# Optimization experiments

Hardware: AMD Instinct MI355X
Metric: run time of the kernel (lower is better)

Reference implementation:

```python
import jax, jax.numpy as jnp
import numpy as np
from jax import lax

EPS = 1e-5
K = 16

def bn(x, g, b):
    # BatchNorm2d in training mode: biased batch stats over (B,H,W)
    m = x.mean(axis=(0, 2, 3), keepdims=True)
    v = x.var(axis=(0, 2, 3), keepdims=True)
    return (x - m) * lax.rsqrt(v + EPS) * g.reshape(1, -1, 1, 1) + b.reshape(1, -1, 1, 1)

def lrelu(x):
    return jnp.where(x >= 0, x, 0.01 * x)

def conv1x1(x, w, b):  # x:[B,C,N,K], w:[O,C]
    return jnp.einsum('bcnk,oc->bonk', x, w) + b.reshape(1, -1, 1, 1)

def edge_features_xyz(x, pc, k):
    B, C, N = x.shape
    xt = jnp.swapaxes(x, 1, 2)                      # [B,N,C]
    xs = jnp.sum(xt * xt, axis=2, keepdims=True)    # [B,N,1]
    dist = -2.0 * jnp.einsum('bnc,bcm->bnm', xt, x) + xs + jnp.swapaxes(xs, 1, 2)
    idx = jnp.argsort(dist, axis=2)[:, :, 1:k + 1]  # [B,N,k] skip self
    gather = jax.vmap(lambda fb, ib: fb[:, ib])     # [C,N],[N,k]->[C,N,k]
    nb = gather(x, idx)                             # [B,C,N,k]
    nb_xyz = gather(pc, idx)                        # [B,3,N,k]
    central = jnp.broadcast_to(x[..., None], (B, C, N, k))
    central_xyz = jnp.broadcast_to(pc[..., None], (B, 3, N, k))
    e_fea = jnp.concatenate([central, nb - central], axis=1)          # [B,2C,N,k]
    e_xyz = jnp.concatenate([central_xyz, nb_xyz - central_xyz], axis=1)  # [B,6,N,k]
    return e_fea, e_xyz

def forward(x, pc, fea_w, fea_b, fea_g, fea_be, xyz_w, xyz_b, xyz_g, xyz_be,
            all1_w, all1_b, all1_g, all1_be, all2_w, all2_b, all2_g, all2_be,
            inte_w, inte_b, inte_g, inte_be, c2_w, c2_b, c2_g, c2_be):
    B, Fin, N = x.shape
    k = K
    e_fea, e_xyz = edge_features_xyz(x, pc, k)      # [B,2Fin,N,k],[B,6,N,k]
    w_fea = lrelu(bn(conv1x1(e_fea, fea_w, fea_b), fea_g, fea_be))   # [B,16,N,k]
    w_xyz = lrelu(bn(conv1x1(e_xyz, xyz_w, xyz_b), xyz_g, xyz_be))   # [B,16,N,k]
    w = w_fea * w_xyz
    w = lrelu(bn(conv1x1(w, all1_w, all1_b), all1_g, all1_be))       # [B,64,N,k]
    w = lrelu(bn(conv1x1(w, all2_w, all2_b), all2_g, all2_be))       # [B,2Fin,N,k]
    w = jax.nn.softmax(w, axis=-1)
    CC = 2 * Fin
    # inte_conv_hk: Conv2d(2Fin->4Fin, kernel [1, k//2+1]) -> [B,4Fin,N,k//2]
    inte = lax.conv_general_dilated(e_fea, inte_w, (1, 1), 'VALID',
                                    dimension_numbers=('NCHW', 'OIHW', 'NCHW'))
    inte = inte + inte_b.reshape(1, -1, 1, 1)
    inte = lrelu(bn(inte, inte_g, inte_be))
    # torch reshape dance: [B,4Fin,N,k/2] -> [B,N,4Fin,k/2] -> [B,N,2Fin,2,k/2] -> [B,N,2Fin,k] -> [B,2Fin,N,k]
    inte = jnp.transpose(inte, (0, 2, 1, 3)).reshape(B, N, CC, 2, k // 2)
    inte = inte.reshape(B, N, CC, k).transpose(0, 2, 1, 3)
    inte_x = inte * w
    merge = jnp.concatenate([e_fea, inte_x], axis=3)                 # [B,2Fin,N,2k]
    # conv2: kernel [1,2k] spans full width -> contraction
    out = jnp.einsum('bcnw,ocw->bon', merge, c2_w[:, :, 0, :]) + c2_b.reshape(1, -1, 1)
    out = out[..., None]                                             # [B,2Fout,N,1]
    out = jnp.maximum(bn(out, c2_g, c2_be), 0.0)                     # ReLU
    Fout = out.shape[1] // 2
    return out.reshape(B, Fout, 2 * N)

def setup_inputs():
    B, Fin, Fout, N, k = 8, 64, 64, 2048, 16
    ks = jax.random.split(jax.random.key(0), 10)
    p = lambda i, s, sc=0.05: jax.random.normal(ks[i], s, jnp.float32) * sc
    return {
        'x': p(0, (B, Fin, N), 1.0),
        'pc': p(1, (B, 3, N), 1.0),
        'fea_w': p(2, (16, 2 * Fin)), 'fea_b': jnp.zeros(16), 'fea_g': jnp.ones(16), 'fea_be': jnp.zeros(16),
        'xyz_w': p(3, (16, 6)), 'xyz_b': jnp.zeros(16), 'xyz_g': jnp.ones(16), 'xyz_be': jnp.zeros(16),
        'all1_w': p(4, (64, 16)), 'all1_b': jnp.zeros(64), 'all1_g': jnp.ones(64), 'all1_be': jnp.zeros(64),
        'all2_w': p(5, (2 * Fin, 64)), 'all2_b': jnp.zeros(2 * Fin), 'all2_g': jnp.ones(2 * Fin), 'all2_be': jnp.zeros(2 * Fin),
        'inte_w': p(6, (4 * Fin, 2 * Fin, 1, k // 2 + 1)), 'inte_b': jnp.zeros(4 * Fin), 'inte_g': jnp.ones(4 * Fin), 'inte_be': jnp.zeros(4 * Fin),
        'c2_w': p(7, (2 * Fout, 2 * Fin, 1, 2 * k)), 'c2_b': jnp.zeros(2 * Fout), 'c2_g': jnp.ones(2 * Fout), 'c2_be': jnp.zeros(2 * Fout),
    }

def reference(x, pc, fea_w, fea_b, fea_g, fea_be, xyz_w, xyz_b, xyz_g, xyz_be,
              all1_w, all1_b, all1_g, all1_be, all2_w, all2_b, all2_g, all2_be,
              inte_w, inte_b, inte_g, inte_be, c2_w, c2_b, c2_g, c2_be):
    return forward(x, pc, fea_w, fea_b, fea_g, fea_be, xyz_w, xyz_b, xyz_g, xyz_be,
                   all1_w, all1_b, all1_g, all1_be, all2_w, all2_b, all2_g, all2_be,
                   inte_w, inte_b, inte_g, inte_be, c2_w, c2_b, c2_g, c2_be)
```

## Files before the change

kernel.cpp:

```cpp
#include <hip/hip_runtime.h>
#include <math.h>

typedef unsigned short ushort_t;

#define B_   8
#define N_   2048
#define K_   16
#define C2_  128
#define C4_  256
#define KH_  8
#define TAP_ 9
#define NK_  32768
#define EPSv 1e-5f
#define BIGF 3.0e38f
#define NMASK 2047

constexpr size_t AL(size_t x) { return (x + 255) & ~(size_t)255; }
constexpr size_t OFF_XT   = 0;
constexpr size_t OFF_IDX  = OFF_XT  + AL(4ull * B_ * N_ * 64);
constexpr size_t OFF_U1   = OFF_IDX + AL(4ull * B_ * N_ * K_);
constexpr size_t OFF_V1   = OFF_U1  + AL(4ull * B_ * 16 * N_);
constexpr size_t OFF_U2   = OFF_V1  + AL(4ull * B_ * N_ * 16);
constexpr size_t OFF_V2   = OFF_U2  + AL(4ull * B_ * 16 * N_);
constexpr size_t OFF_S    = OFF_V2  + AL(4ull * B_ * N_ * 16);
constexpr size_t OFF_P    = OFF_S   + AL(4ull * B_ * N_ * C2_);
constexpr size_t OFF_W1   = OFF_P   + AL(4ull * B_ * N_ * C4_);
constexpr size_t OFF_QB   = OFF_W1  + AL(4ull * B_ * 16 * NK_);
constexpr size_t OFF_ITB  = OFF_QB  + AL(2ull * (size_t)B_ * N_ * TAP_ * C4_);
constexpr size_t OFF_A4B  = OFF_ITB + AL(2ull * (size_t)B_ * N_ * 2048);
constexpr size_t OFF_M    = OFF_A4B + AL(2ull * (size_t)B_ * N_ * 2048);
constexpr size_t OFF_PART = OFF_M   + AL(2ull * (size_t)B_ * N_ * 2048);
constexpr size_t OFF_OUT2 = OFF_PART+ AL(4ull * 2 * (size_t)B_ * N_ * C2_);
constexpr size_t OFF_WQ2  = OFF_OUT2+ AL(4ull * B_ * N_ * C2_);
constexpr size_t OFF_WC2  = OFF_WQ2 + AL(4ull * TAP_ * C4_ * 64);
constexpr size_t OFF_WP2  = OFF_WC2 + AL(4ull * 3072 * C2_);
constexpr size_t OFF_WS2  = OFF_WP2 + AL(4ull * C4_ * 64);
constexpr size_t OFF_WU12 = OFF_WS2 + AL(4ull * C2_ * 64);
constexpr size_t OFF_WV12 = OFF_WU12+ AL(4ull * 16 * 64);
constexpr size_t OFF_WU22 = OFF_WV12+ AL(4ull * 16 * 64);
constexpr size_t OFF_WV22 = OFF_WU22+ AL(4ull * 64);
constexpr size_t OFF_A12  = OFF_WV22+ AL(4ull * 64);
constexpr size_t OFF_A22  = OFF_A12 + AL(4ull * 64 * 16);
constexpr size_t OFF_ST   = OFF_A22 + AL(4ull * C2_ * 64);
constexpr size_t OFF_PROG = OFF_ST  + AL(4ull * 4096);
constexpr size_t POOL_SZ  = OFF_PROG + AL(4ull * 64);

static char* g_pool_mem = nullptr;
struct PoolInit {
  PoolInit() { if (hipMalloc((void**)&g_pool_mem, POOL_SZ) != hipSuccess) g_pool_mem = nullptr; }
};
static PoolInit g_pool_init;

#define ST_S1S 0
#define ST_S1Q 16
#define ST_S2S 32
#define ST_S2Q 48
#define ST_S5S 64
#define ST_S5Q 320
#define ST_S4S 576
#define ST_S4Q 704
#define ST_S6S 832
#define ST_S6Q 960
#define ST_B1SC 1088
#define ST_B1SH 1104
#define ST_B2SC 1120
#define ST_B2SH 1136
#define ST_B3SC 1152
#define ST_B3SH 1216
#define ST_B4SC 1280
#define ST_B4SH 1408
#define ST_B5SC 1536
#define ST_B5SH 1792
#define ST_B6SC 2048
#define ST_B6SH 2176
#define ST_S3M  2304
#define ST_S3V  2440

#define BASE(b)  char* bb = (b)
#define P_XT   ((float*)(bb + OFF_XT))
#define P_IDX  ((int*)(bb + OFF_IDX))
#define P_U1   ((float*)(bb + OFF_U1))
#define P_V1   ((float*)(bb + OFF_V1))
#define P_U2   ((float*)(bb + OFF_U2))
#define P_V2   ((float*)(bb + OFF_V2))
#define P_Sb   ((float*)(bb + OFF_S))
#define P_P    ((float*)(bb + OFF_P))
#define P_W1   ((float*)(bb + OFF_W1))
#define P_QB   ((ushort_t*)(bb + OFF_QB))
#define P_IT   ((ushort_t*)(bb + OFF_ITB))
#define P_A4   ((ushort_t*)(bb + OFF_A4B))
#define P_M    ((ushort_t*)(bb + OFF_M))
#define P_PART ((float*)(bb + OFF_PART))
#define P_OUT2 ((float*)(bb + OFF_OUT2))
#define P_WQ2  ((float*)(bb + OFF_WQ2))
#define P_WC2  ((float*)(bb + OFF_WC2))
#define P_WP2  ((float*)(bb + OFF_WP2))
#define P_WS2  ((float*)(bb + OFF_WS2))
#define P_WU12 ((float*)(bb + OFF_WU12))
#define P_WV12 ((float*)(bb + OFF_WV12))
#define P_WU22 ((float*)(bb + OFF_WU22))
#define P_WV22 ((float*)(bb + OFF_WV22))
#define P_A12  ((float*)(bb + OFF_A12))
#define P_A22  ((float*)(bb + OFF_A22))
#define P_ST   ((float*)(bb + OFF_ST))
#define P_PROG ((int*)(bb + OFF_PROG))

#define PROG(id) do { if (threadIdx.x == 0) atomicAdd(&P_PROG[(id)], 1); } while (0)

static __device__ __forceinline__ float lrelu(float x) { return x >= 0.0f ? x : 0.01f * x; }
static __device__ __forceinline__ float bf2f(unsigned h) {
  union { float f; unsigned u; } v; v.u = h << 16; return v.f;
}
static __device__ __forceinline__ ushort_t f2bf(float f) {
  union { float f; unsigned u; } v; v.f = f;
  unsigned r = v.u + 0x7fffu + ((v.u >> 16) & 1u);
  return (ushort_t)(r >> 16);
}

__global__ __launch_bounds__(256) void zero_kernel(char* base)
{
  BASE(base);
  for (int i = threadIdx.x; i < 4096; i += 256) P_ST[i] = 0.0f;
  for (int i = threadIdx.x; i < 64; i += 256) P_PROG[i] = 0;
  __syncthreads();
  if (threadIdx.x == 0) P_PROG[0] = 1;
}

__global__ __launch_bounds__(256) void xt_kernel(char* base, const float* __restrict__ x)
{
  BASE(base);
  PROG(8);
  int b = blockIdx.x >> 5; int m0 = (blockIdx.x & 31) * 64;
  int t = threadIdx.x;
  __shared__ float tile[64 * 65];
  for (int i = t; i < 4096; i += 256) {
    int ml = i & 63, c = i >> 6;
    tile[c * 65 + ml] = x[((size_t)(b * 64 + c)) * N_ + m0 + ml];
  }
  __syncthreads();
  for (int i = t; i < 4096; i += 256) {
    int c = i & 63, ml = i >> 6;
    P_XT[((size_t)(b * N_) + m0 + ml) * 64 + c] = tile[c * 65 + ml];
  }
}

__global__ __launch_bounds__(256) void prep_kernel(char* base,
    const float* __restrict__ fea_w,
    const float* __restrict__ xyz_w, const float* __restrict__ inte_w,
    const float* __restrict__ c2_w, const float* __restrict__ all1_w,
    const float* __restrict__ all2_w)
{
  BASE(base);
  PROG(1);
  int i = blockIdx.x * 256 + threadIdx.x;
  if (i < 1024) { int o = i & 15, c = i >> 4;
    P_WU12[i] = fea_w[o * 128 + c] - fea_w[o * 128 + 64 + c]; return; }
  i -= 1024;
  if (i < 1024) { int o = i & 15, c = i >> 4;
    P_WV12[i] = fea_w[o * 128 + 64 + c]; return; }
  i -= 1024;
  if (i < 64) { int c = i & 3, o = i >> 2;
    P_WU22[i] = (c < 3) ? (xyz_w[o * 6 + c] - xyz_w[o * 6 + 3 + c]) : 0.0f; return; }
  i -= 64;
  if (i < 64) { int c = i & 3, o = i >> 2;
    P_WV22[i] = (c < 3) ? xyz_w[o * 6 + 3 + c] : 0.0f; return; }
  i -= 64;
  if (i < 16384) { int o = i & 255, c = i >> 8;
    float s = 0.0f;
    for (int t = 0; t < TAP_; t++)
      s += inte_w[(o * 128 + c) * TAP_ + t] - inte_w[(o * 128 + 64 + c) * TAP_ + t];
    P_WP2[i] = s; return; }
  i -= 16384;
  if (i < 147456) {
    int o = i & 255; int tc = i >> 8; int c = tc & 63; int tt = tc >> 6;
    P_WQ2[i] = inte_w[(o * 128 + 64 + c) * TAP_ + tt]; return; }
  i -= 147456;
  if (i < 8192) { int o = i & 127, c = i >> 7;
    float s = 0.0f;
    for (int p = 0; p < 16; p++)
      s += c2_w[(o * 128 + c) * 32 + p] - c2_w[(o * 128 + 64 + c) * 32 + p];
    P_WS2[i] = s; return; }
  i -= 8192;
  if (i < 393216) { int o = i & 127; int k = i >> 7; float v;
    if (k < 1024) { int c = k >> 4, p = k & 15; v = c2_w[(o * 128 + 64 + c) * 32 + p]; }
    else { int kr = k - 1024; int cc = kr >> 4, kk = kr & 15; v = c2_w[(o * 128 + cc) * 32 + 16 + kk]; }
    P_WC2[i] = v; return; }
  i -= 393216;
  if (i < 1024) { int c = i & 15, o = i >> 4; P_A12[i] = all1_w[o * 16 + c]; return; }
  i -= 1024;
  if (i < 8192) {
    int o = i & 127, c = i >> 7; P_A22[i] = all2_w[o * 64 + c]; return; }
}

__global__ __launch_bounds__(256) void phaseA_kernel(char* base,
                                                     const float* __restrict__ x,
                                                     const float* __restrict__ pc)
{
  BASE(base);
  PROG(2);
  __shared__ __align__(16) char smem[33824];
  int bid = blockIdx.x;
  int t = threadIdx.x;
  if (bid % 5 != 0) {
    int kb = bid - bid / 5 - 1;
    int b = kb >> 9; int n0 = (kb & 511) * 4;
    float (*sdist)[N_] = (float(*)[N_])smem;
    float (*xn)[64]    = (float(*)[64])(smem + 32768);
    float* sxn         = (float*)(smem + 32768 + 1024);
    {
      int nn = t >> 6, c = t & 63;
      xn[nn][c] = P_XT[((size_t)(b * N_) + n0 + nn) * 64 + c];
    }
    __syncthreads();
    if (t < 4) {
      float s = 0.0f;
      for (int c = 0; c < 64; c++) { float v = xn[t][c]; s += v * v; }
      sxn[t] = s;
    }
    __syncthreads();
    float dd[32]; float xs[8];
#pragma unroll
    for (int i = 0; i < 32; i++) dd[i] = 0.0f;
#pragma unroll
    for (int i = 0; i < 8; i++) xs[i] = 0.0f;
    const float* xbase = x + (size_t)b * 64 * N_ + (t << 3);
    for (int cq = 0; cq < 16; cq++) {
      float4 a0 = *(const float4*)&xn[0][cq * 4];
      float4 a1 = *(const float4*)&xn[1][cq * 4];
      float4 a2 = *(const float4*)&xn[2][cq * 4];
      float4 a3 = *(const float4*)&xn[3][cq * 4];
      float p[4][8];
#pragma unroll
      for (int cc = 0; cc < 4; cc++) {
        const float* xr = xbase + (size_t)(cq * 4 + cc) * N_;
        float4 u = *(const float4*)xr;
        float4 v = *(const float4*)(xr + 4);
        p[cc][0] = u.x; p[cc][1] = u.y; p[cc][2] = u.z; p[cc][3] = u.w;
        p[cc][4] = v.x; p[cc][5] = v.y; p[cc][6] = v.z; p[cc][7] = v.w;
      }
#pragma unroll
      for (int j = 0; j < 8; j++) {
        float x0 = p[0][j], x1 = p[1][j], x2 = p[2][j], x3 = p[3][j];
        xs[j] += x0 * x0 + x1 * x1 + x2 * x2 + x3 * x3;
        dd[0 * 8 + j] += a0.x * x0 + a0.y * x1 + a0.z * x2 + a0.w * x3;
        dd[1 * 8 + j] += a1.x * x0 + a1.y * x1 + a1.z * x2 + a1.w * x3;
        dd[2 * 8 + j] += a2.x * x0 + a2.y * x1 + a2.z * x2 + a2.w * x3;
        dd[3 * 8 + j] += a3.x * x0 + a3.y * x1 + a3.z * x2 + a3.w * x3;
      }
    }
    float sx0 = sxn[0], sx1 = sxn[1], sx2 = sxn[2], sx3 = sxn[3];
    int mb = t << 3;
#pragma unroll
    for (int j = 0; j < 8; j++) {
      int m = mb + j;
      float d0 = -2.0f * dd[0 * 8 + j] + sx0 + xs[j];
      float d1 = -2.0f * dd[1 * 8 + j] + sx1 + xs[j];
      float d2 = -2.0f * dd[2 * 8 + j] + sx2 + xs[j];
      float d3 = -2.0f * dd[3 * 8 + j] + sx3 + xs[j];
      sdist[0][m] = (m == n0 + 0) ? BIGF : d0;
      sdist[1][m] = (m == n0 + 1) ? BIGF : d1;
      sdist[2][m] = (m == n0 + 2) ? BIGF : d2;
      sdist[3][m] = (m == n0 + 3) ? BIGF : d3;
    }
    __syncthreads();
    int ln = t & 63; int wv = t >> 6;
    float v[32];
#pragma unroll
    for (int j = 0; j < 32; j++) v[j] = sdist[wv][ln + j * 64];
    float bv = v[0]; int bj = 0;
#pragma unroll
    for (int j = 1; j < 32; j++) { if (v[j] < bv) { bv = v[j]; bj = j; } }
    int* op = P_IDX + ((size_t)(b * N_) + n0 + wv) * K_;
    for (int it = 0; it < K_; it++) {
      float rv = bv; int ri = ln + (bj << 6);
#pragma unroll
      for (int off = 32; off > 0; off >>= 1) {
        float ov = __shfl_xor(rv, off);
        int oi = __shfl_xor(ri, off);
        if (ov < rv || (ov == rv && oi < ri)) { rv = ov; ri = oi; }
      }
      if (ln == 0) op[it] = ri;
      if ((ri & 63) == ln) {
        int slot = ri >> 6;
#pragma unroll
        for (int j = 0; j < 32; j++) v[j] = (j == slot) ? BIGF : v[j];
        bv = v[0]; bj = 0;
#pragma unroll
        for (int j = 1; j < 32; j++) { if (v[j] < bv) { bv = v[j]; bj = j; } }
      }
    }
    return;
  }
  int s = bid / 5;
  if (s < 512) {
    int b = s >> 6; int m0 = (s & 63) * 32;
    float (*actS)[40] = (float(*)[40])smem;
    float (*pcs)[32]  = (float(*)[32])(smem + 10240);
    for (int i = t; i < 2048; i += 256) {
      int c = i & 63, mm = i >> 6;
      actS[c][mm] = P_XT[((size_t)(b * N_) + m0 + mm) * 64 + c];
    }
    if (t < 96) {
      int c = t >> 5, mm = t & 31;
      pcs[c][mm] = pc[(b * 3 + c) * N_ + m0 + mm];
    }
    __syncthreads();
    size_t bN = (size_t)(b * N_);
    {
      int og = t & 31, pg = t >> 5;
      float acc[8][4];
#pragma unroll
      for (int oi = 0; oi < 8; oi++)
#pragma unroll
        for (int pj = 0; pj < 4; pj++) acc[oi][pj] = 0.0f;
      for (int c = 0; c < 64; c++) {
        float4 a = *(const float4*)&actS[c][pg * 4];
        const float* wr = P_WP2 + c * 256 + og * 8;
        float4 w0 = *(const float4*)wr;
        float4 w1 = *(const float4*)(wr + 4);
        float av[4] = {a.x, a.y, a.z, a.w};
        float wv[8] = {w0.x, w0.y, w0.z, w0.w, w1.x, w1.y, w1.z, w1.w};
#pragma unroll
        for (int oi = 0; oi < 8; oi++)
#pragma unroll
          for (int pj = 0; pj < 4; pj++) acc[oi][pj] += wv[oi] * av[pj];
      }
#pragma unroll
      for (int pj = 0; pj < 4; pj++) {
        float* pp = P_P + (bN + m0 + pg * 4 + pj) * C4_ + og * 8;
        *(float4*)pp = make_float4(acc[0][pj], acc[1][pj], acc[2][pj], acc[3][pj]);
        *(float4*)(pp + 4) = make_float4(acc[4][pj], acc[5][pj], acc[6][pj], acc[7][pj]);
      }
    }
    {
      int og = t & 15, pg = t >> 4;
      float acc[8][2];
#pragma unroll
      for (int oi = 0; oi < 8; oi++) { acc[oi][0] = 0.0f; acc[oi][1] = 0.0f; }
      for (int c = 0; c < 64; c++) {
        float a0 = actS[c][pg * 2], a1 = actS[c][pg * 2 + 1];
        const float* wr = P_WS2 + c * 128 + og * 8;
        float4 w0 = *(const float4*)wr;
        float4 w1 = *(const float4*)(wr + 4);
        float wv[8] = {w0.x, w0.y, w0.z, w0.w, w1.x, w1.y, w1.z, w1.w};
#pragma unroll
        for (int oi = 0; oi < 8; oi++) { acc[oi][0] += wv[oi] * a0; acc[oi][1] += wv[oi] * a1; }
      }
#pragma unroll
      for (int pj = 0; pj < 2; pj++) {
        float* sp = P_Sb + (bN + m0 + pg * 2 + pj) * C2_ + og * 8;
        *(float4*)sp = make_float4(acc[0][pj], acc[1][pj], acc[2][pj], acc[3][pj]);
        *(float4*)(sp + 4) = make_float4(acc[4][pj], acc[5][pj], acc[6][pj], acc[7][pj]);
      }
    }
    {
      int o = t & 15, pg = t >> 4;
      float aU[2] = {0.0f, 0.0f}, aV[2] = {0.0f, 0.0f};
      for (int c = 0; c < 64; c++) {
        float wu = P_WU12[c * 16 + o];
        float wv = P_WV12[c * 16 + o];
        float a0 = actS[c][pg * 2], a1 = actS[c][pg * 2 + 1];
        aU[0] += wu * a0; aU[1] += wu * a1;
        aV[0] += wv * a0; aV[1] += wv * a1;
      }
      float u0 = P_WU22[o * 4], u1 = P_WU22[o * 4 + 1], u2w = P_WU22[o * 4 + 2];
      float v0 = P_WV22[o * 4], v1 = P_WV22[o * 4 + 1], v2w = P_WV22[o * 4 + 2];
#pragma unroll
      for (int pj = 0; pj < 2; pj++) {
        int m = m0 + pg * 2 + pj;
        P_U1[((b * 16 + o) << 11) + m] = aU[pj];
        P_V1[(bN + m) * 16 + o] = aV[pj];
        float p0 = pcs[0][pg * 2 + pj], p1 = pcs[1][pg * 2 + pj], p2 = pcs[2][pg * 2 + pj];
        P_U2[((b * 16 + o) << 11) + m] = u0 * p0 + u1 * p1 + u2w * p2;
        P_V2[(bN + m) * 16 + o] = v0 * p0 + v1 * p1 + v2w * p2;
      }
    }
    return;
  }
  {
    int q = s - 512;
    int b = q >> 6; int m0 = (q & 63) * 32;
    float (*actS)[40] = (float(*)[40])smem;
    for (int i = t; i < 2048; i += 256) {
      int c = i & 63, mm = i >> 6;
      actS[c][mm] = P_XT[((size_t)(b * N_) + m0 + mm) * 64 + c];
    }
    __syncthreads();
    int og = t & 31;
    int pg = t >> 5;
    int m = m0 + pg * 4;
    for (int t9 = 0; t9 < TAP_; t9++) {
      const float* wbase = P_WQ2 + ((size_t)t9 * 64) * 256 + og * 8;
      float acc[8][4];
#pragma unroll
      for (int oi = 0; oi < 8; oi++)
#pragma unroll
        for (int pj = 0; pj < 4; pj++) acc[oi][pj] = 0.0f;
      for (int kc = 0; kc < 64; kc++) {
        float4 a = *(const float4*)&actS[kc][pg * 4];
        const float* wr = wbase + (size_t)kc * 256;
        float4 w0 = *(const float4*)wr;
        float4 w1 = *(const float4*)(wr + 4);
        float av[4] = {a.x, a.y, a.z, a.w};
        float wv[8] = {w0.x, w0.y, w0.z, w0.w, w1.x, w1.y, w1.z, w1.w};
#pragma unroll
        for (int oi = 0; oi < 8; oi++)
#pragma unroll
          for (int pj = 0; pj < 4; pj++)
            acc[oi][pj] += wv[oi] * av[pj];
      }
#pragma unroll
      for (int pj = 0; pj < 4; pj++) {
        ushort_t* qp = P_QB + ((size_t)(b * N_ + m + pj) * TAP_ + t9) * C4_ + og * 8;
        unsigned u0 = (unsigned)f2bf(acc[0][pj]) | ((unsigned)f2bf(acc[1][pj]) << 16);
        unsigned u1 = (unsigned)f2bf(acc[2][pj]) | ((unsigned)f2bf(acc[3][pj]) << 16);
        unsigned u2 = (unsigned)f2bf(acc[4][pj]) | ((unsigned)f2bf(acc[5][pj]) << 16);
        unsigned u3 = (unsigned)f2bf(acc[6][pj]) | ((unsigned)f2bf(acc[7][pj]) << 16);
        *(uint4*)qp = make_uint4(u0, u1, u2, u3);
      }
    }
    return;
  }
}

__global__ __launch_bounds__(256) void phaseB_kernel(char* base,
                                                     const float* __restrict__ inte_b,
                                                     const float* __restrict__ fea_b,
                                                     const float* __restrict__ xyz_b)
{
  BASE(base);
  PROG(15);
  __shared__ __align__(16) char smem[1024];
  int bid = blockIdx.x;
  int t = threadIdx.x;
  if (bid % 5 != 0) {
    int kb = bid - bid / 5 - 1;
    int b = kb >> 9; int n0 = (kb & 511) * 4;
    int o = t;
    int (*sidx)[16] = (int(*)[16])smem;
    if (t < 64) sidx[t >> 4][t & 15] = P_IDX[((size_t)(b * N_) + n0 + (t >> 4)) * K_ + (t & 15)] & NMASK;
    __syncthreads();
    float bias = inte_b[o];
    float ssum = 0.0f, ssq = 0.0f;
    for (int nn = 0; nn < 4; nn++) {
      int n = n0 + nn;
      float bse = bias + P_P[((size_t)(b * N_) + n) * C4_ + o];
      float acc[8];
#pragma unroll
      for (int j = 0; j < 8; j++) acc[j] = bse;
      for (int p = 0; p < 16; p++) {
        const ushort_t* qr = P_QB + (size_t)(b * N_ + sidx[nn][p]) * TAP_ * C4_ + o;
#pragma unroll
        for (int tt = 0; tt < TAP_; tt++) {
          int j = p - tt;
          if (j >= 0 && j < 8) acc[j] += bf2f(((unsigned)qr[tt * C4_]) << 16 >> 16 << 16 >> 16);
        }
      }
      ushort_t* ip = P_IT + ((size_t)(b * N_) + n) * 2048 + o * 8;
#pragma unroll
      for (int j = 0; j < 8; j++) { float v = acc[j]; ip[j] = f2bf(v); ssum += v; ssq += v * v; }
    }
    atomicAdd(&P_ST[ST_S5S + o], ssum);
    atomicAdd(&P_ST[ST_S5Q + o], ssq);
    return;
  }
  {
    int s = bid / 5;
    int b = s >> 7; int n0 = (s & 127) * 16;
    int o = t & 15; int kk = t >> 4;
    float* red = (float*)smem;
    float fb = fea_b[o], xb = xyz_b[o];
    float s1 = 0, q1 = 0, s2 = 0, q2 = 0;
    for (int nn = 0; nn < 16; nn++) {
      int n = n0 + nn;
      int m = P_IDX[((b << 11) + n) * K_ + kk] & NMASK;
      float a1 = fb + P_U1[((b * 16 + o) << 11) + n] + P_V1[(((size_t)(b << 11) + m) << 4) + o];
      s1 += a1; q1 += a1 * a1;
      float a2 = xb + P_U2[((b * 16 + o) << 11) + n] + P_V2[(((size_t)(b << 11) + m) << 4) + o];
      s2 += a2; q2 += a2 * a2;
    }
    red[t] = s1; __syncthreads();
    if (t < 16) { float s = 0; for (int k2 = 0; k2 < 16; k2++) s += red[k2 * 16 + t]; atomicAdd(&P_ST[ST_S1S + t], s); }
    __syncthreads();
    red[t] = q1; __syncthreads();
    if (t < 16) { float s = 0; for (int k2 = 0; k2 < 16; k2++) s += red[k2 * 16 + t]; atomicAdd(&P_ST[ST_S1Q + t], s); }
    __syncthreads();
    red[t] = s2; __syncthreads();
    if (t < 16) { float s = 0; for (int k2 = 0; k2 < 16; k2++) s += red[k2 * 16 + t]; atomicAdd(&P_ST[ST_S2S + t], s); }
    __syncthreads();
    red[t] = q2; __syncthreads();
    if (t < 16) { float s = 0; for (int k2 = 0; k2 < 16; k2++) s += red[k2 * 16 + t]; atomicAdd(&P_ST[ST_S2Q + t], s); }
    return;
  }
}

__global__ __launch_bounds__(256) void finalize_bn_kernel(char* base,
                                   const float* __restrict__ g,
                                   const float* __restrict__ be,
                                   int sum_off, int sq_off, int sc_off, int sh_off,
                                   int nch, float inv_cnt, int kid)
{
  BASE(base);
  PROG(kid);
  int i = threadIdx.x;
  if (i < nch) {
    float mu = P_ST[sum_off + i] * inv_cnt;
    float var = fmaxf(P_ST[sq_off + i] * inv_cnt - mu * mu, 0.0f);
    float s = g[i] * rsqrtf(var + EPSv);
    P_ST[sc_off + i] = s; P_ST[sh_off + i] = be[i] - mu * s;
  }
}

__global__ __launch_bounds__(256) void w1_kernel(char* base,
    const float* __restrict__ fea_b, const float* __restrict__ xyz_b)
{
  BASE(base);
  PROG(7);
  int b = blockIdx.x >> 7; int n0 = (blockIdx.x & 127) * 16;
  int t = threadIdx.x;
  __shared__ int sidx[16 * 16];
  __shared__ __align__(16) float ol[16 * 260];
  {
    int nl = t >> 4, k = t & 15;
    sidx[nl * 16 + k] = P_IDX[((size_t)((b << 11) + n0 + nl)) * 16 + k] & NMASK;
  }
  __syncthreads();
  int c = t >> 4; int nl = t & 15; int n = n0 + nl;
  float u1 = P_U1[((b * 16 + c) << 11) + n];
  float u2 = P_U2[((b * 16 + c) << 11) + n];
  float c1 = fea_b[c] + u1, c2v = xyz_b[c] + u2;
  float s1 = P_ST[ST_B1SC + c], h1 = P_ST[ST_B1SH + c];
  float s2 = P_ST[ST_B2SC + c], h2 = P_ST[ST_B2SH + c];
  float o16[16];
#pragma unroll
  for (int kk = 0; kk < 16; kk++) {
    int m = sidx[nl * 16 + kk];
    float a1 = c1 + P_V1[(((size_t)(b << 11) + m) << 4) + c];
    a1 = lrelu(a1 * s1 + h1);
    float a2 = c2v + P_V2[(((size_t)(b << 11) + m) << 4) + c];
    a2 = lrelu(a2 * s2 + h2);
    o16[kk] = a1 * a2;
  }
  float* wp = P_W1 + ((size_t)(b * 16 + c)) * NK_ + ((size_t)n << 4);
#pragma unroll
  for (int j = 0; j < 4; j++)
    *(float4*)(wp + j * 4) = make_float4(o16[4 * j], o16[4 * j + 1], o16[4 * j + 2], o16[4 * j + 3]);
  float* orow = ol + c * 260 + nl * 16;
#pragma unroll
  for (int j = 0; j < 4; j++)
    *(float4*)(orow + j * 4) = make_float4(o16[4 * j], o16[4 * j + 1], o16[4 * j + 2], o16[4 * j + 3]);
  __syncthreads();
  if (t < 136) {
    int cc1 = 0, rem = t;
    while (rem >= 16 - cc1) { rem -= 16 - cc1; cc1++; }
    int cc2 = cc1 + rem;
    const float* r1 = ol + cc1 * 260;
    const float* r2 = ol + cc2 * 260;
    float acc = 0.0f;
    for (int e = 0; e < 256; e += 4) {
      float4 xv = *(const float4*)(r1 + e);
      float4 yv = *(const float4*)(r2 + e);
      acc += xv.x * yv.x + xv.y * yv.y + xv.z * yv.z + xv.w * yv.w;
    }
    atomicAdd(&P_ST[ST_S3M + t], acc);
  } else if (t < 152) {
    const float* r = ol + (t - 136) * 260;
    float acc = 0.0f;
    for (int e = 0; e < 256; e += 4) {
      float4 xv = *(const float4*)(r + e);
      acc += xv.x + xv.y + xv.z + xv.w;
    }
    atomicAdd(&P_ST[ST_S3V + t - 136], acc);
  }
}

__global__ __launch_bounds__(256) void finalize_bn3_kernel(char* base,
                                    const float* __restrict__ b1,
                                    const float* __restrict__ g,
                                    const float* __restrict__ be)
{
  BASE(base);
  PROG(9);
  int o = threadIdx.x;
  if (o >= 64) return;
  float A[16];
  for (int c = 0; c < 16; c++) A[c] = P_A12[o * 16 + c];
  float dv = 0.0f;
  for (int c = 0; c < 16; c++) dv += A[c] * P_ST[ST_S3V + c];
  float quad = 0.0f; int p = 0;
  for (int c1 = 0; c1 < 16; c1++)
    for (int c2 = c1; c2 < 16; c2++) {
      float m = P_ST[ST_S3M + p]; p++;
      quad += (c1 == c2 ? 1.0f : 2.0f) * A[c1] * A[c2] * m;
    }
  float bo = b1[o];
  const float inv = 1.0f / 262144.0f;
  float mean = dv * inv + bo;
  float e2 = quad * inv + 2.0f * bo * dv * inv + bo * bo;
  float var = fmaxf(e2 - mean * mean, 0.0f);
  float s = g[o] * rsqrtf(var + EPSv);
  P_ST[ST_B3SC + o] = s; P_ST[ST_B3SH + o] = be[o] - mean * s;
}

__global__ __launch_bounds__(256) void a4_kernel(char* base,
                                                 const float* __restrict__ all1_b,
                                                 const float* __restrict__ all2_b)
{
  BASE(base);
  PROG(10);
  int b = blockIdx.x >> 9; int col0 = (blockIdx.x & 511) * 64;
  int t = threadIdx.x;
  __shared__ float sw[16 * 68];
  __shared__ __align__(16) float hS[64 * 68];
  for (int i = t; i < 1024; i += 256) {
    int c = i >> 6, l = i & 63;
    sw[c * 68 + l] = P_W1[((size_t)(b * 16 + c)) * NK_ + col0 + l];
  }
  __syncthreads();
  {
    int col = t & 63; int q = t >> 6;
    float in16[16];
#pragma unroll
    for (int c = 0; c < 16; c++) in16[c] = sw[c * 68 + col];
    for (int oo = 0; oo < 16; oo++) {
      int o = q * 16 + oo;
      const float* wr = P_A12 + o * 16;
      float a = all1_b[o];
#pragma unroll
      for (int c = 0; c < 16; c++) a += wr[c] * in16[c];
      hS[o * 68 + col] = lrelu(a * P_ST[ST_B3SC + o] + P_ST[ST_B3SH + o]);
    }
  }
  __syncthreads();
  int cg = t & 15;
  int og = t >> 4;
  float acc[8][4];
#pragma unroll
  for (int oi = 0; oi < 8; oi++) {
    float bo = all2_b[og * 8 + oi];
#pragma unroll
    for (int cj = 0; cj < 4; cj++) acc[oi][cj] = bo;
  }
  for (int hk = 0; hk < 64; hk++) {
    float4 hv = *(const float4*)&hS[hk * 68 + cg * 4];
    const float* wr = P_A22 + hk * 128 + og * 8;
    float4 w0 = *(const float4*)wr;
    float4 w1 = *(const float4*)(wr + 4);
    float av[4] = {hv.x, hv.y, hv.z, hv.w};
    float wv[8] = {w0.x, w0.y, w0.z, w0.w, w1.x, w1.y, w1.z, w1.w};
#pragma unroll
    for (int oi = 0; oi < 8; oi++)
#pragma unroll
      for (int cj = 0; cj < 4; cj++)
        acc[oi][cj] += wv[oi] * av[cj];
  }
  int colb = col0 + cg * 4;
  int n = colb >> 4; int kk0 = colb & 15;
  ushort_t* dst = P_A4 + ((size_t)(b * N_) + n) * 2048 + kk0;
  float psum[8], qsum[8];
#pragma unroll
  for (int oi = 0; oi < 8; oi++) {
    int o = og * 8 + oi;
    unsigned lo = (unsigned)f2bf(acc[oi][0]) | ((unsigned)f2bf(acc[oi][1]) << 16);
    unsigned hi = (unsigned)f2bf(acc[oi][2]) | ((unsigned)f2bf(acc[oi][3]) << 16);
    *(uint2*)(dst + o * 16) = make_uint2(lo, hi);
    float r0 = bf2f(lo & 0xffffu), r1 = bf2f(lo >> 16);
    float r2 = bf2f(hi & 0xffffu), r3 = bf2f(hi >> 16);
    psum[oi] = r0 + r1 + r2 + r3;
    qsum[oi] = r0 * r0 + r1 * r1 + r2 * r2 + r3 * r3;
  }
  __syncthreads();
  float* redS = hS;
#pragma unroll
  for (int oi = 0; oi < 8; oi++) redS[(og * 8 + oi) * 16 + cg] = psum[oi];
  __syncthreads();
  if (t < 128) {
    float s = 0.0f;
    for (int j = 0; j < 16; j++) s += redS[t * 16 + j];
    atomicAdd(&P_ST[ST_S4S + t], s);
  }
  __syncthreads();
#pragma unroll
  for (int oi = 0; oi < 8; oi++) redS[(og * 8 + oi) * 16 + cg] = qsum[oi];
  __syncthreads();
  if (t < 128) {
    float s = 0.0f;
    for (int j = 0; j < 16; j++) s += redS[t * 16 + j];
    atomicAdd(&P_ST[ST_S4Q + t], s);
  }
}

__global__ __launch_bounds__(256) void softfuse_kernel(char* base)
{
  BASE(base);
  PROG(13);
  int rid = blockIdx.x * 256 + threadIdx.x;
  int cc = rid & 127; int r = rid >> 7;
  float s = P_ST[ST_B4SC + cc], h = P_ST[ST_B4SH + cc];
  size_t base_off = (size_t)r * 2048 + cc * 16;
  const ushort_t* pa = P_A4 + base_off;
  uint4 u0 = *(const uint4*)pa;
  uint4 u1 = *(const uint4*)(pa + 8);
  unsigned ws[8] = {u0.x, u0.y, u0.z, u0.w, u1.x, u1.y, u1.z, u1.w};
  float v[16];
#pragma unroll
  for (int j = 0; j < 8; j++) {
    union { float f; unsigned u; } lo, hi;
    lo.u = ws[j] << 16; hi.u = ws[j] & 0xffff0000u;
    v[2 * j] = lo.f; v[2 * j + 1] = hi.f;
  }
  float mx = -BIGF;
#pragma unroll
  for (int i = 0; i < 16; i++) {
    float y = lrelu(v[i] * s + h);
    v[i] = y; mx = fmaxf(mx, y);
  }
  float sum = 0.0f;
#pragma unroll
  for (int i = 0; i < 16; i++) { float e = expf(v[i] - mx); v[i] = e; sum += e; }
  float inv = (sum > 0.0f) ? 1.0f / sum : 0.0f;
#pragma unroll
  for (int i = 0; i < 16; i++) v[i] = bf2f((unsigned)f2bf(v[i] * inv));
  float s5a = P_ST[ST_B5SC + cc * 2],     h5a = P_ST[ST_B5SH + cc * 2];
  float s5b = P_ST[ST_B5SC + cc * 2 + 1], h5b = P_ST[ST_B5SH + cc * 2 + 1];
  const ushort_t* itp = P_IT + base_off;
  uint4 i0 = *(const uint4*)itp;
  uint4 i1 = *(const uint4*)(itp + 8);
  unsigned iw[8] = {i0.x, i0.y, i0.z, i0.w, i1.x, i1.y, i1.z, i1.w};
  unsigned mw[8];
#pragma unroll
  for (int j = 0; j < 8; j++) {
    union { float f; unsigned u; } il, ih;
    il.u = iw[j] << 16; ih.u = iw[j] & 0xffff0000u;
    float s5 = (j < 4) ? s5a : s5b;
    float h5 = (j < 4) ? h5a : h5b;
    float m0 = lrelu(il.f * s5 + h5) * v[2 * j];
    float m1 = lrelu(ih.f * s5 + h5) * v[2 * j + 1];
    mw[j] = (unsigned)f2bf(m0) | ((unsigned)f2bf(m1) << 16);
  }
  ushort_t* mp = P_M + base_off;
  *(uint4*)mp = make_uint4(mw[0], mw[1], mw[2], mw[3]);
  *(uint4*)(mp + 8) = make_uint4(mw[4], mw[5], mw[6], mw[7]);
}

__global__ __launch_bounds__(256) void final_conv_kernel(char* base)
{
  BASE(base);
  PROG(17);
  int ks = blockIdx.x & 1;
  int tile = (blockIdx.x >> 1) & 31; int b = blockIdx.x >> 6;
  int n0 = tile * 64;
  int t = threadIdx.x;
  int cg4 = (t & 15) * 4;
  int obase = (t >> 4) * 8;
  __shared__ __align__(16) float tileS[128 * 68];
  __shared__ int sidxT[16 * 64];
  for (int i = t; i < 1024; i += 256) {
    int cl = i & 63, p = i >> 6;
    sidxT[p * 64 + cl] = P_IDX[((size_t)(b * N_) + n0 + cl) * K_ + p] & NMASK;
  }
  float acc[32];
#pragma unroll
  for (int i = 0; i < 32; i++) acc[i] = 0.0f;
  int kbeg = ks * 1536;
  for (int k0 = kbeg; k0 < kbeg + 1536; k0 += 128) {
    __syncthreads();
    if (k0 < 1024) {
      int c0 = k0 >> 4;
      int cl = t & 63; int pg = t >> 6;
      for (int pp = 0; pp < 4; pp++) {
        int p = pg * 4 + pp;
        int m = sidxT[p * 64 + cl];
        const float* xp = P_XT + ((size_t)(b * N_) + m) * 64 + c0;
        float4 v0 = *(const float4*)xp;
        float4 v1 = *(const float4*)(xp + 4);
        tileS[(0 * 16 + p) * 68 + cl] = v0.x;
        tileS[(1 * 16 + p) * 68 + cl] = v0.y;
        tileS[(2 * 16 + p) * 68 + cl] = v0.z;
        tileS[(3 * 16 + p) * 68 + cl] = v0.w;
        tileS[(4 * 16 + p) * 68 + cl] = v1.x;
        tileS[(5 * 16 + p) * 68 + cl] = v1.y;
        tileS[(6 * 16 + p) * 68 + cl] = v1.z;
        tileS[(7 * 16 + p) * 68 + cl] = v1.w;
      }
    } else {
      int cl = t & 63; int kg = t >> 6;
      size_t rb = ((size_t)(b * N_) + n0 + cl) * 2048 + (size_t)(k0 - 1024) + kg * 32;
      const ushort_t* mp = P_M + rb;
      for (int j8 = 0; j8 < 4; j8++) {
        uint4 u = *(const uint4*)(mp + j8 * 8);
        unsigned ws[4] = {u.x, u.y, u.z, u.w};
#pragma unroll
        for (int q = 0; q < 4; q++) {
          union { float f; unsigned uu; } lo, hi;
          lo.uu = ws[q] << 16; hi.uu = ws[q] & 0xffff0000u;
          int kc = kg * 32 + j8 * 8 + q * 2;
          tileS[kc * 68 + cl] = lo.f;
          tileS[(kc + 1) * 68 + cl] = hi.f;
        }
      }
    }
    __syncthreads();
    for (int kc = 0; kc < 128; kc++) {
      float4 a = *(const float4*)&tileS[kc * 68 + cg4];
      const float* wr = P_WC2 + (size_t)(k0 + kc) * C2_ + obase;
      float4 w0 = *(const float4*)wr;
      float4 w1 = *(const float4*)(wr + 4);
      float av[4] = {a.x, a.y, a.z, a.w};
      float wv[8] = {w0.x, w0.y, w0.z, w0.w, w1.x, w1.y, w1.z, w1.w};
#pragma unroll
      for (int oi = 0; oi < 8; oi++)
#pragma unroll
        for (int cj = 0; cj < 4; cj++)
          acc[oi * 4 + cj] += wv[oi] * av[cj];
    }
  }
#pragma unroll
  for (int cj = 0; cj < 4; cj++) {
    float* op = P_PART + ((size_t)ks * B_ * N_ + (size_t)b * N_ + n0 + cg4 + cj) * C2_ + obase;
    *(float4*)op = make_float4(acc[0 * 4 + cj], acc[1 * 4 + cj], acc[2 * 4 + cj], acc[3 * 4 + cj]);
    *(float4*)(op + 4) = make_float4(acc[4 * 4 + cj], acc[5 * 4 + cj], acc[6 * 4 + cj], acc[7 * 4 + cj]);
  }
}

__global__ __launch_bounds__(256) void reduce_stats_kernel(char* base,
                                                           const float* __restrict__ c2_b)
{
  BASE(base);
  PROG(18);
  int r0 = blockIdx.x * 32;
  int t = threadIdx.x; int o = t & 127; int h = t >> 7;
  const size_t STRIDE = (size_t)B_ * N_ * C2_;
  float cb = c2_b[o];
  float s = 0, q = 0;
  for (int r = r0 + h; r < r0 + 32; r += 2) {
    size_t off = (size_t)r * C2_ + o;
    float v = cb + P_Sb[off] + P_PART[off] + P_PART[STRIDE + off];
    P_OUT2[off] = v;
    s += v; q += v * v;
  }
  __shared__ float rs[256], rq[256];
  rs[t] = s; rq[t] = q; __syncthreads();
  if (t < 128) {
    atomicAdd(&P_ST[ST_S6S + o], rs[t] + rs[t + 128]);
    atomicAdd(&P_ST[ST_S6Q + o], rq[t] + rq[t + 128]);
  }
}

__global__ __launch_bounds__(256) void output_kernel(char* base, float* __restrict__ out)
{
  BASE(base);
  PROG(20);
  int b = blockIdx.x >> 6; int n0 = (blockIdx.x & 63) * 32;
  int t = threadIdx.x;
  __shared__ float tile[32 * 133];
  for (int i = t; i < 4096; i += 256) {
    int o = i & 127, nl = i >> 7;
    float v = P_OUT2[((size_t)(b * N_) + n0 + nl) * C2_ + o];
    v = v * P_ST[ST_B6SC + o] + P_ST[ST_B6SH + o];
    tile[nl * 133 + o] = fmaxf(v, 0.0f);
  }
  __syncthreads();
  for (int i = t; i < 4096; i += 256) {
    int nl = i & 31, o = i >> 5;
    out[(((size_t)b * 64 + (o >> 1)) * 2 + (o & 1)) * 2048 + n0 + nl] = tile[nl * 133 + o];
  }
}

__global__ void diag_kernel(char* base, float* __restrict__ out)
{
  BASE(base);
  const int expctd[22] = {1, 2253, 5120, 0, 0, 1, 1, 1024, 256, 1, 4096,
                          0, 1, 8192, 0, 5120, 1, 512, 512, 1, 512, 0};
  int t = threadIdx.x;
  int bad = 99;
  if (t < 22 && P_PROG[t] != expctd[t]) bad = t;
#pragma unroll
  for (int off = 32; off > 0; off >>= 1) {
    int ob = __shfl_xor(bad, off);
    if (ob < bad) bad = ob;
  }
  if (t == 0 && bad != 99) out[0] = 100.0f + 10.0f * (float)bad;
}

__global__ void code_kernel(float* __restrict__ out, float code)
{
  if (threadIdx.x == 0 && blockIdx.x == 0) out[0] = code;
}

extern "C" void kernel_launch(void* const* d_in, const int* in_sizes, int n_in,
                              void* d_out, int out_size, void* d_ws, size_t ws_size,
                              hipStream_t stream) {
  const float* x      = (const float*)d_in[0];
  const float* pc     = (const float*)d_in[1];
  const float* fea_w  = (const float*)d_in[2];
  const float* fea_b  = (const float*)d_in[3];
  const float* fea_g  = (const float*)d_in[4];
  const float* fea_be = (const float*)d_in[5];
  const float* xyz_w  = (const float*)d_in[6];
  const float* xyz_b  = (const float*)d_in[7];
  const float* xyz_g  = (const float*)d_in[8];
  const float* xyz_be = (const float*)d_in[9];
  const float* all1_w = (const float*)d_in[10];
  const float* all1_b = (const float*)d_in[11];
  const float* all1_g = (const float*)d_in[12];
  const float* all1_be= (const float*)d_in[13];
  const float* all2_w = (const float*)d_in[14];
  const float* all2_b = (const float*)d_in[15];
  const float* all2_g = (const float*)d_in[16];
  const float* all2_be= (const float*)d_in[17];
  const float* inte_w = (const float*)d_in[18];
  const float* inte_b = (const float*)d_in[19];
  const float* inte_g = (const float*)d_in[20];
  const float* inte_be= (const float*)d_in[21];
  const float* c2_w   = (const float*)d_in[22];
  const float* c2_b   = (const float*)d_in[23];
  const float* c2_g   = (const float*)d_in[24];
  const float* c2_be  = (const float*)d_in[25];
  float* out = (float*)d_out;
  (void)in_sizes; (void)n_in; (void)out_size; (void)d_ws; (void)ws_size;

  if (g_pool_mem == nullptr) {
    code_kernel<<<1, 64, 0, stream>>>(out, 500.0f);
    return;
  }
  char* base = g_pool_mem;

  zero_kernel<<<1, 256, 0, stream>>>(base);
  xt_kernel<<<256, 256, 0, stream>>>(base, x);
  prep_kernel<<<2253, 256, 0, stream>>>(base, fea_w, xyz_w, inte_w, c2_w, all1_w, all2_w);
  phaseA_kernel<<<5120, 256, 0, stream>>>(base, x, pc);
  phaseB_kernel<<<5120, 256, 0, stream>>>(base, inte_b, fea_b, xyz_b);
  finalize_bn_kernel<<<1, 256, 0, stream>>>(base, fea_g, fea_be, ST_S1S, ST_S1Q, ST_B1SC, ST_B1SH, 16, 1.0f / 262144.0f, 5);
  finalize_bn_kernel<<<1, 256, 0, stream>>>(base, xyz_g, xyz_be, ST_S2S, ST_S2Q, ST_B2SC, ST_B2SH, 16, 1.0f / 262144.0f, 6);
  finalize_bn_kernel<<<1, 256, 0, stream>>>(base, inte_g, inte_be, ST_S5S, ST_S5Q, ST_B5SC, ST_B5SH, 256, 1.0f / 131072.0f, 16);
  w1_kernel<<<1024, 256, 0, stream>>>(base, fea_b, xyz_b);
  finalize_bn3_kernel<<<1, 256, 0, stream>>>(base, all1_b, all1_g, all1_be);
  a4_kernel<<<4096, 256, 0, stream>>>(base, all1_b, all2_b);
  finalize_bn_kernel<<<1, 256, 0, stream>>>(base, all2_g, all2_be, ST_S4S, ST_S4Q, ST_B4SC, ST_B4SH, 128, 1.0f / 262144.0f, 12);
  softfuse_kernel<<<8192, 256, 0, stream>>>(base);
  final_conv_kernel<<<512, 256, 0, stream>>>(base);
  reduce_stats_kernel<<<512, 256, 0, stream>>>(base, c2_b);
  finalize_bn_kernel<<<1, 256, 0, stream>>>(base, c2_g, c2_be, ST_S6S, ST_S6Q, ST_B6SC, ST_B6SH, 128, 1.0f / 16384.0f, 19);
  output_kernel<<<512, 256, 0, stream>>>(base, out);
  diag_kernel<<<1, 64, 0, stream>>>(base, out);
}
```

Before: 1.160 ms.

## Move gathered-neighbor part of final conv into a4 kernel launch

The first 1024 reduction channels of the final conv, which depend only on gathered neighbor features and not on the softmax output, are computed by extra blocks interleaved into the a4 launch (every 17th block). The final conv then only handles the softmax-weighted part, split into two equal halves, and a third partial buffer is summed in the stats reduction. The aim is to overlap the gather-heavy work with the a4 stage and balance the final conv's split, at the cost of more shared memory per block in phaseC and an extra partial buffer read.

```diff
diff --git a/kernel.cpp b/kernel.cpp
--- a/kernel.cpp
+++ b/kernel.cpp
@@ -30,7 +30,7 @@
 constexpr size_t OFF_A4B  = OFF_ITB + AL(2ull * (size_t)B_ * N_ * 2048);
 constexpr size_t OFF_M    = OFF_A4B + AL(2ull * (size_t)B_ * N_ * 2048);
 constexpr size_t OFF_PART = OFF_M   + AL(2ull * (size_t)B_ * N_ * 2048);
-constexpr size_t OFF_OUT2 = OFF_PART+ AL(4ull * 2 * (size_t)B_ * N_ * C2_);
+constexpr size_t OFF_OUT2 = OFF_PART+ AL(4ull * 3 * (size_t)B_ * N_ * C2_);
 constexpr size_t OFF_WQ2  = OFF_OUT2+ AL(4ull * B_ * N_ * C2_);
 constexpr size_t OFF_WC2  = OFF_WQ2 + AL(4ull * TAP_ * C4_ * 64);
 constexpr size_t OFF_WP2  = OFF_WC2 + AL(4ull * 3072 * C2_);
@@ -602,91 +602,156 @@
   P_ST[ST_B3SC + o] = s; P_ST[ST_B3SH + o] = be[o] - mean * s;
 }
 
-__global__ __launch_bounds__(256) void a4_kernel(char* base,
-                                                 const float* __restrict__ all1_b,
-                                                 const float* __restrict__ all2_b)
+__global__ __launch_bounds__(256) void phaseC_kernel(char* base,
+                                                     const float* __restrict__ all1_b,
+                                                     const float* __restrict__ all2_b)
 {
   BASE(base);
   PROG(10);
-  int b = blockIdx.x >> 9; int col0 = (blockIdx.x & 511) * 64;
+  __shared__ __align__(16) char smem[38912];
+  int bid = blockIdx.x;
   int t = threadIdx.x;
-  __shared__ float sw[16 * 68];
-  __shared__ __align__(16) float hS[64 * 68];
-  for (int i = t; i < 1024; i += 256) {
-    int c = i >> 6, l = i & 63;
-    sw[c * 68 + l] = P_W1[((size_t)(b * 16 + c)) * NK_ + col0 + l];
-  }
-  __syncthreads();
+  if (bid % 17 == 0) {
+    int s = bid / 17;
+    int tile = s & 31; int b = s >> 5;
+    int n0 = tile * 64;
+    int cg4 = (t & 15) * 4;
+    int obase = (t >> 4) * 8;
+    float* tileS = (float*)smem;
+    int* sidxT = (int*)(smem + 34816);
+    for (int i = t; i < 1024; i += 256) {
+      int cl = i & 63, p = i >> 6;
+      sidxT[p * 64 + cl] = P_IDX[((size_t)(b * N_) + n0 + cl) * K_ + p] & NMASK;
+    }
+    float acc[32];
+#pragma unroll
+    for (int i = 0; i < 32; i++) acc[i] = 0.0f;
+    for (int k0 = 0; k0 < 1024; k0 += 128) {
+      __syncthreads();
+      {
+        int c0 = k0 >> 4;
+        int cl = t & 63; int pg = t >> 6;
+        for (int pp = 0; pp < 4; pp++) {
+          int p = pg * 4 + pp;
+          int m = sidxT[p * 64 + cl];
+          const float* xp = P_XT + ((size_t)(b * N_) + m) * 64 + c0;
+          float4 v0 = *(const float4*)xp;
+          float4 v1 = *(const float4*)(xp + 4);
+          tileS[(0 * 16 + p) * 68 + cl] = v0.x;
+          tileS[(1 * 16 + p) * 68 + cl] = v0.y;
+          tileS[(2 * 16 + p) * 68 + cl] = v0.z;
+          tileS[(3 * 16 + p) * 68 + cl] = v0.w;
+          tileS[(4 * 16 + p) * 68 + cl] = v1.x;
+          tileS[(5 * 16 + p) * 68 + cl] = v1.y;
+          tileS[(6 * 16 + p) * 68 + cl] = v1.z;
+          tileS[(7 * 16 + p) * 68 + cl] = v1.w;
+        }
+      }
+      __syncthreads();
+      for (int kc = 0; kc < 128; kc++) {
+        float4 a = *(const float4*)&tileS[kc * 68 + cg4];
+        const float* wr = P_WC2 + (size_t)(k0 + kc) * C2_ + obase;
+        float4 w0 = *(const float4*)wr;
+        float4 w1 = *(const float4*)(wr + 4);
+        float av[4] = {a.x, a.y, a.z, a.w};
+        float wv[8] = {w0.x, w0.y, w0.z, w0.w, w1.x, w1.y, w1.z, w1.w};
+#pragma unroll
+        for (int oi = 0; oi < 8; oi++)
+#pragma unroll
+          for (int cj = 0; cj < 4; cj++)
+            acc[oi * 4 + cj] += wv[oi] * av[cj];
+      }
+    }
+#pragma unroll
+    for (int cj = 0; cj < 4; cj++) {
+      float* op = P_PART + ((size_t)b * N_ + n0 + cg4 + cj) * C2_ + obase;
+      *(float4*)op = make_float4(acc[0 * 4 + cj], acc[1 * 4 + cj], acc[2 * 4 + cj], acc[3 * 4 + cj]);
+      *(float4*)(op + 4) = make_float4(acc[4 * 4 + cj], acc[5 * 4 + cj], acc[6 * 4 + cj], acc[7 * 4 + cj]);
+    }
+    return;
+  }
   {
-    int col = t & 63; int q = t >> 6;
-    float in16[16];
-#pragma unroll
-    for (int c = 0; c < 16; c++) in16[c] = sw[c * 68 + col];
-    for (int oo = 0; oo < 16; oo++) {
-      int o = q * 16 + oo;
-      const float* wr = P_A12 + o * 16;
-      float a = all1_b[o];
-#pragma unroll
-      for (int c = 0; c < 16; c++) a += wr[c] * in16[c];
-      hS[o * 68 + col] = lrelu(a * P_ST[ST_B3SC + o] + P_ST[ST_B3SH + o]);
-    }
-  }
-  __syncthreads();
-  int cg = t & 15;
-  int og = t >> 4;
-  float acc[8][4];
-#pragma unroll
-  for (int oi = 0; oi < 8; oi++) {
-    float bo = all2_b[og * 8 + oi];
-#pragma unroll
-    for (int cj = 0; cj < 4; cj++) acc[oi][cj] = bo;
-  }
-  for (int hk = 0; hk < 64; hk++) {
-    float4 hv = *(const float4*)&hS[hk * 68 + cg * 4];
-    const float* wr = P_A22 + hk * 128 + og * 8;
-    float4 w0 = *(const float4*)wr;
-    float4 w1 = *(const float4*)(wr + 4);
-    float av[4] = {hv.x, hv.y, hv.z, hv.w};
-    float wv[8] = {w0.x, w0.y, w0.z, w0.w, w1.x, w1.y, w1.z, w1.w};
-#pragma unroll
-    for (int oi = 0; oi < 8; oi++)
-#pragma unroll
-      for (int cj = 0; cj < 4; cj++)
-        acc[oi][cj] += wv[oi] * av[cj];
-  }
-  int colb = col0 + cg * 4;
-  int n = colb >> 4; int kk0 = colb & 15;
-  ushort_t* dst = P_A4 + ((size_t)(b * N_) + n) * 2048 + kk0;
-  float psum[8], qsum[8];
-#pragma unroll
-  for (int oi = 0; oi < 8; oi++) {
-    int o = og * 8 + oi;
-    unsigned lo = (unsigned)f2bf(acc[oi][0]) | ((unsigned)f2bf(acc[oi][1]) << 16);
-    unsigned hi = (unsigned)f2bf(acc[oi][2]) | ((unsigned)f2bf(acc[oi][3]) << 16);
-    *(uint2*)(dst + o * 16) = make_uint2(lo, hi);
-    float r0 = bf2f(lo & 0xffffu), r1 = bf2f(lo >> 16);
-    float r2 = bf2f(hi & 0xffffu), r3 = bf2f(hi >> 16);
-    psum[oi] = r0 + r1 + r2 + r3;
-    qsum[oi] = r0 * r0 + r1 * r1 + r2 * r2 + r3 * r3;
-  }
-  __syncthreads();
-  float* redS = hS;
-#pragma unroll
-  for (int oi = 0; oi < 8; oi++) redS[(og * 8 + oi) * 16 + cg] = psum[oi];
-  __syncthreads();
-  if (t < 128) {
-    float s = 0.0f;
-    for (int j = 0; j < 16; j++) s += redS[t * 16 + j];
-    atomicAdd(&P_ST[ST_S4S + t], s);
-  }
-  __syncthreads();
-#pragma unroll
-  for (int oi = 0; oi < 8; oi++) redS[(og * 8 + oi) * 16 + cg] = qsum[oi];
-  __syncthreads();
-  if (t < 128) {
-    float s = 0.0f;
-    for (int j = 0; j < 16; j++) s += redS[t * 16 + j];
-    atomicAdd(&P_ST[ST_S4Q + t], s);
+    int kb = bid - bid / 17 - 1;
+    int b = kb >> 9; int col0 = (kb & 511) * 64;
+    float* sw = (float*)smem;
+    float* hS = (float*)(smem + 4352);
+    for (int i = t; i < 1024; i += 256) {
+      int c = i >> 6, l = i & 63;
+      sw[c * 68 + l] = P_W1[((size_t)(b * 16 + c)) * NK_ + col0 + l];
+    }
+    __syncthreads();
+    {
+      int col = t & 63; int q = t >> 6;
+      float in16[16];
+#pragma unroll
+      for (int c = 0; c < 16; c++) in16[c] = sw[c * 68 + col];
+      for (int oo = 0; oo < 16; oo++) {
+        int o = q * 16 + oo;
+        const float* wr = P_A12 + o * 16;
+        float a = all1_b[o];
+#pragma unroll
+        for (int c = 0; c < 16; c++) a += wr[c] * in16[c];
+        hS[o * 68 + col] = lrelu(a * P_ST[ST_B3SC + o] + P_ST[ST_B3SH + o]);
+      }
+    }
+    __syncthreads();
+    int cg = t & 15;
+    int og = t >> 4;
+    float acc[8][4];
+#pragma unroll
+    for (int oi = 0; oi < 8; oi++) {
+      float bo = all2_b[og * 8 + oi];
+#pragma unroll
+      for (int cj = 0; cj < 4; cj++) acc[oi][cj] = bo;
+    }
+    for (int hk = 0; hk < 64; hk++) {
+      float4 hv = *(const float4*)&hS[hk * 68 + cg * 4];
+      const float* wr = P_A22 + hk * 128 + og * 8;
+      float4 w0 = *(const float4*)wr;
+      float4 w1 = *(const float4*)(wr + 4);
+      float av[4] = {hv.x, hv.y, hv.z, hv.w};
+      float wv[8] = {w0.x, w0.y, w0.z, w0.w, w1.x, w1.y, w1.z, w1.w};
+#pragma unroll
+      for (int oi = 0; oi < 8; oi++)
+#pragma unroll
+        for (int cj = 0; cj < 4; cj++)
+          acc[oi][cj] += wv[oi] * av[cj];
+    }
+    int colb = col0 + cg * 4;
+    int n = colb >> 4; int kk0 = colb & 15;
+    ushort_t* dst = P_A4 + ((size_t)(b * N_) + n) * 2048 + kk0;
+    float psum[8], qsum[8];
+#pragma unroll
+    for (int oi = 0; oi < 8; oi++) {
+      int o = og * 8 + oi;
+      unsigned lo = (unsigned)f2bf(acc[oi][0]) | ((unsigned)f2bf(acc[oi][1]) << 16);
+      unsigned hi = (unsigned)f2bf(acc[oi][2]) | ((unsigned)f2bf(acc[oi][3]) << 16);
+      *(uint2*)(dst + o * 16) = make_uint2(lo, hi);
+      float r0 = bf2f(lo & 0xffffu), r1 = bf2f(lo >> 16);
+      float r2 = bf2f(hi & 0xffffu), r3 = bf2f(hi >> 16);
+      psum[oi] = r0 + r1 + r2 + r3;
+      qsum[oi] = r0 * r0 + r1 * r1 + r2 * r2 + r3 * r3;
+    }
+    __syncthreads();
+    float* redS = hS;
+#pragma unroll
+    for (int oi = 0; oi < 8; oi++) redS[(og * 8 + oi) * 16 + cg] = psum[oi];
+    __syncthreads();
+    if (t < 128) {
+      float s = 0.0f;
+      for (int j = 0; j < 16; j++) s += redS[t * 16 + j];
+      atomicAdd(&P_ST[ST_S4S + t], s);
+    }
+    __syncthreads();
+#pragma unroll
+    for (int oi = 0; oi < 8; oi++) redS[(og * 8 + oi) * 16 + cg] = qsum[oi];
+    __syncthreads();
+    if (t < 128) {
+      float s = 0.0f;
+      for (int j = 0; j < 16; j++) s += redS[t * 16 + j];
+      atomicAdd(&P_ST[ST_S4Q + t], s);
+    }
+    return;
   }
 }
 
@@ -754,36 +819,13 @@
   int cg4 = (t & 15) * 4;
   int obase = (t >> 4) * 8;
   __shared__ __align__(16) float tileS[128 * 68];
-  __shared__ int sidxT[16 * 64];
-  for (int i = t; i < 1024; i += 256) {
-    int cl = i & 63, p = i >> 6;
-    sidxT[p * 64 + cl] = P_IDX[((size_t)(b * N_) + n0 + cl) * K_ + p] & NMASK;
-  }
   float acc[32];
 #pragma unroll
   for (int i = 0; i < 32; i++) acc[i] = 0.0f;
-  int kbeg = ks * 1536;
-  for (int k0 = kbeg; k0 < kbeg + 1536; k0 += 128) {
-    __syncthreads();
-    if (k0 < 1024) {
-      int c0 = k0 >> 4;
-      int cl = t & 63; int pg = t >> 6;
-      for (int pp = 0; pp < 4; pp++) {
-        int p = pg * 4 + pp;
-        int m = sidxT[p * 64 + cl];
-        const float* xp = P_XT + ((size_t)(b * N_) + m) * 64 + c0;
-        float4 v0 = *(const float4*)xp;
-        float4 v1 = *(const float4*)(xp + 4);
-        tileS[(0 * 16 + p) * 68 + cl] = v0.x;
-        tileS[(1 * 16 + p) * 68 + cl] = v0.y;
-        tileS[(2 * 16 + p) * 68 + cl] = v0.z;
-        tileS[(3 * 16 + p) * 68 + cl] = v0.w;
-        tileS[(4 * 16 + p) * 68 + cl] = v1.x;
-        tileS[(5 * 16 + p) * 68 + cl] = v1.y;
-        tileS[(6 * 16 + p) * 68 + cl] = v1.z;
-        tileS[(7 * 16 + p) * 68 + cl] = v1.w;
-      }
-    } else {
+  int kbeg = 1024 + ks * 1024;
+  for (int k0 = kbeg; k0 < kbeg + 1024; k0 += 128) {
+    __syncthreads();
+    {
       int cl = t & 63; int kg = t >> 6;
       size_t rb = ((size_t)(b * N_) + n0 + cl) * 2048 + (size_t)(k0 - 1024) + kg * 32;
       const ushort_t* mp = P_M + rb;
@@ -817,7 +859,7 @@
   }
 #pragma unroll
   for (int cj = 0; cj < 4; cj++) {
-    float* op = P_PART + ((size_t)ks * B_ * N_ + (size_t)b * N_ + n0 + cg4 + cj) * C2_ + obase;
+    float* op = P_PART + ((size_t)(1 + ks) * B_ * N_ + (size_t)b * N_ + n0 + cg4 + cj) * C2_ + obase;
     *(float4*)op = make_float4(acc[0 * 4 + cj], acc[1 * 4 + cj], acc[2 * 4 + cj], acc[3 * 4 + cj]);
     *(float4*)(op + 4) = make_float4(acc[4 * 4 + cj], acc[5 * 4 + cj], acc[6 * 4 + cj], acc[7 * 4 + cj]);
   }
@@ -835,7 +877,8 @@
   float s = 0, q = 0;
   for (int r = r0 + h; r < r0 + 32; r += 2) {
     size_t off = (size_t)r * C2_ + o;
-    float v = cb + P_Sb[off] + P_PART[off] + P_PART[STRIDE + off];
+    float v = cb + P_Sb[off] + P_PART[off] + P_PART[STRIDE + off]
+            + P_PART[2 * STRIDE + off];
     P_OUT2[off] = v;
     s += v; q += v * v;
   }
@@ -870,7 +913,7 @@
 __global__ void diag_kernel(char* base, float* __restrict__ out)
 {
   BASE(base);
-  const int expctd[22] = {1, 2253, 5120, 0, 0, 1, 1, 1024, 256, 1, 4096,
+  const int expctd[22] = {1, 2253, 5120, 0, 0, 1, 1, 1024, 256, 1, 4352,
                           0, 1, 8192, 0, 5120, 1, 512, 512, 1, 512, 0};
   int t = threadIdx.x;
   int bad = 99;
@@ -936,7 +979,7 @@
   finalize_bn_kernel<<<1, 256, 0, stream>>>(base, inte_g, inte_be, ST_S5S, ST_S5Q, ST_B5SC, ST_B5SH, 256, 1.0f / 131072.0f, 16);
   w1_kernel<<<1024, 256, 0, stream>>>(base, fea_b, xyz_b);
   finalize_bn3_kernel<<<1, 256, 0, stream>>>(base, all1_b, all1_g, all1_be);
-  a4_kernel<<<4096, 256, 0, stream>>>(base, all1_b, all2_b);
+  phaseC_kernel<<<4352, 256, 0, stream>>>(base, all1_b, all2_b);
   finalize_bn_kernel<<<1, 256, 0, stream>>>(base, all2_g, all2_be, ST_S4S, ST_S4Q, ST_B4SC, ST_B4SH, 128, 1.0f / 262144.0f, 12);
   softfuse_kernel<<<8192, 256, 0, stream>>>(base);
   final_conv_kernel<<<512, 256, 0, stream>>>(base);
```

Result: slower. 1.219 ms (+5.1%).
